# Kernel optimization log

Measured on AMD Instinct MI355X. Metric: run time of the kernel, lower is better.

Reference implementation:

```python
import jax, jax.numpy as jnp
import numpy as np

B, T, D = 32, 1024, 768
H = 768          # GRU hidden size
INNER = 512      # fc output size
NOUT = 39        # out_proj outputs (13 classes x 3 ACCDOA coords)


def setup_inputs() -> dict:
    key = jax.random.key(0)
    ks = jax.random.split(key, 16)
    s_in = 1.0 / np.sqrt(H)
    inp = {
        "features": jax.random.normal(ks[0], (B, T, D), jnp.float32),
        "padding_mask": jnp.zeros((B, T), jnp.bool_),
        # GRU layer 0 (input D -> H), PyTorch gate order [r, z, n]
        "w_ih0": jax.random.uniform(ks[1], (3 * H, D), jnp.float32, -s_in, s_in),
        "w_hh0": jax.random.uniform(ks[2], (3 * H, H), jnp.float32, -s_in, s_in),
        "b_ih0": jax.random.uniform(ks[3], (3 * H,), jnp.float32, -s_in, s_in),
        "b_hh0": jax.random.uniform(ks[4], (3 * H,), jnp.float32, -s_in, s_in),
        # GRU layer 1 (H -> H)
        "w_ih1": jax.random.uniform(ks[5], (3 * H, H), jnp.float32, -s_in, s_in),
        "w_hh1": jax.random.uniform(ks[6], (3 * H, H), jnp.float32, -s_in, s_in),
        "b_ih1": jax.random.uniform(ks[7], (3 * H,), jnp.float32, -s_in, s_in),
        "b_hh1": jax.random.uniform(ks[8], (3 * H,), jnp.float32, -s_in, s_in),
        # fc: hidden -> inner, then SELU
        "fc_w": jax.random.uniform(ks[9], (INNER, H), jnp.float32, -s_in, s_in),
        "fc_b": jax.random.uniform(ks[10], (INNER,), jnp.float32, -s_in, s_in),
        # out_proj: inner -> num_outs, then tanh
        "out_w": jax.random.uniform(ks[11], (NOUT, INNER), jnp.float32, -1.0 / np.sqrt(INNER), 1.0 / np.sqrt(INNER)),
        "out_b": jax.random.uniform(ks[12], (NOUT,), jnp.float32, -1.0 / np.sqrt(INNER), 1.0 / np.sqrt(INNER)),
    }
    return inp


def _gru_layer(x, w_ih, w_hh, b_ih, b_hh):
    # x: [B, T, Din] -> [B, T, H]; PyTorch GRU math, gate order r,z,n
    b, t, _ = x.shape
    h = w_hh.shape[1]
    # precompute input projections for all timesteps in one big GEMM
    x_proj = jnp.einsum('btd,gd->btg', x, w_ih) + b_ih  # [B, T, 3H]

    def step(h_prev, xp):
        gi_r, gi_z, gi_n = jnp.split(xp, 3, axis=-1)
        gh = h_prev @ w_hh.T + b_hh
        gh_r, gh_z, gh_n = jnp.split(gh, 3, axis=-1)
        r = jax.nn.sigmoid(gi_r + gh_r)
        z = jax.nn.sigmoid(gi_z + gh_z)
        n = jnp.tanh(gi_n + r * gh_n)
        h_new = (1.0 - z) * n + z * h_prev
        return h_new, h_new

    h0 = jnp.zeros((b, h), x.dtype)
    _, ys = jax.lax.scan(step, h0, jnp.swapaxes(x_proj, 0, 1))  # ys: [T, B, H]
    return jnp.swapaxes(ys, 0, 1)


def reference(features, padding_mask, w_ih0, w_hh0, b_ih0, b_hh0,
              w_ih1, w_hh1, b_ih1, b_hh1, fc_w, fc_b, out_w, out_b):
    # dropout_input p=0.0 -> identity (eval); padding_mask unused by forward math
    x = _gru_layer(features, w_ih0, w_hh0, b_ih0, b_hh0)
    x = _gru_layer(x, w_ih1, w_hh1, b_ih1, b_hh1)
    x = jax.nn.selu(x @ fc_w.T + fc_b)          # fc + activation_fn='selu'
    x = jnp.tanh(x @ out_w.T + out_b)           # out_proj + out_activation 'tanh'
    return x
```

## Files before the change

### kernel.cpp

```cpp
#include <hip/hip_runtime.h>
#include <cstdint>

typedef float vf2 __attribute__((ext_vector_type(2)));

#define GB_M 128
#define GB_N 64
#define GB_K 16

__global__ __launch_bounds__(256) void gemm_bt_f32(
    const float* __restrict__ A, const float* __restrict__ B,
    const float* __restrict__ bias, float* __restrict__ C,
    int Mc, int N, int K, int tc_shift, int Tfull, int t0, int act)
{
  __shared__ float As[GB_K][GB_M + 4];
  __shared__ float Bs[GB_K][GB_N + 4];
  const int tid = threadIdx.x;
  const int m0 = blockIdx.y * GB_M;
  const int n0 = blockIdx.x * GB_N;
  const int tx = tid & 15;
  const int ty = tid >> 4;

  const int tcmask = (1 << tc_shift) - 1;
  int arow[2];
#pragma unroll
  for (int i = 0; i < 2; i++) {
    int f = tid + i * 256;
    int row = f >> 2;
    int rc = m0 + row;
    arow[i] = (rc >> tc_shift) * Tfull + t0 + (rc & tcmask);
  }
  const int akq = tid & 3;
  const int brow = tid >> 2;
  const int bn = n0 + brow;

  vf2 acc2[4][4];
#pragma unroll
  for (int i = 0; i < 4; i++)
#pragma unroll
    for (int j = 0; j < 4; j++) acc2[i][j] = (vf2)(0.f);

  for (int k0 = 0; k0 < K; k0 += GB_K) {
#pragma unroll
    for (int i = 0; i < 2; i++) {
      int f = tid + i * 256;
      int row = f >> 2;
      float4 v = *(const float4*)(A + (size_t)arow[i] * K + k0 + akq * 4);
      As[akq * 4 + 0][row] = v.x; As[akq * 4 + 1][row] = v.y;
      As[akq * 4 + 2][row] = v.z; As[akq * 4 + 3][row] = v.w;
    }
    {
      float4 v = make_float4(0.f, 0.f, 0.f, 0.f);
      if (bn < N) v = *(const float4*)(B + (size_t)bn * K + k0 + akq * 4);
      Bs[akq * 4 + 0][brow] = v.x; Bs[akq * 4 + 1][brow] = v.y;
      Bs[akq * 4 + 2][brow] = v.z; Bs[akq * 4 + 3][brow] = v.w;
    }
    __syncthreads();
#pragma unroll
    for (int k = 0; k < GB_K; k++) {
      float4 a0 = *(const float4*)&As[k][ty * 8];
      float4 a1 = *(const float4*)&As[k][ty * 8 + 4];
      float4 b0 = *(const float4*)&Bs[k][tx * 4];
      vf2 a2[4];
      a2[0] = (vf2){a0.x, a0.y}; a2[1] = (vf2){a0.z, a0.w};
      a2[2] = (vf2){a1.x, a1.y}; a2[3] = (vf2){a1.z, a1.w};
      float bv[4] = {b0.x, b0.y, b0.z, b0.w};
#pragma unroll
      for (int j = 0; j < 4; j++) {
        vf2 bs = (vf2){bv[j], bv[j]};
#pragma unroll
        for (int ip = 0; ip < 4; ip++)
          acc2[ip][j] = __builtin_elementwise_fma(a2[ip], bs, acc2[ip][j]);
      }
    }
    __syncthreads();
  }

#pragma unroll
  for (int j = 0; j < 4; j++) {
    int n = n0 + tx * 4 + j;
    if (n >= N) continue;
    float bz = bias[n];
#pragma unroll
    for (int i = 0; i < 8; i++) {
      int m = m0 + ty * 8 + i;
      float x = ((i & 1) ? acc2[i >> 1][j].y : acc2[i >> 1][j].x) + bz;
      if (act == 1) {
        x = 1.0507009873554805f * (x > 0.f ? x : 1.6732632423543772f * (__expf(x) - 1.f));
      } else if (act == 2) {
        x = tanhf(x);
      }
      C[(size_t)m * N + n] = x;
    }
  }
}

#define RT 384
#define RNWG 256

__device__ __forceinline__ void pollge(const unsigned* fp, unsigned want) {
  while (__hip_atomic_load(fp, __ATOMIC_RELAXED, __HIP_MEMORY_SCOPE_AGENT) < want)
    __builtin_amdgcn_s_sleep(1);
}

__global__ __launch_bounds__(RT, 1) void gru_rec(
    const float* __restrict__ gi, const float* __restrict__ w_hh,
    const float* __restrict__ b_hh, float* __restrict__ hb,
    unsigned* __restrict__ flags, float* __restrict__ seq,
    int t0, int Tc)
{
  __shared__ float hs[8][776];
  const int wg = blockIdx.x;
  const int jg = wg & 63;
  const int sd = wg >> 6;
  const int j0 = jg * 12;
  const int tid = threadIdx.x;
  const int p  = tid >> 6;
  const int ks = tid & 63;

  unsigned* flagX_my = flags + (((0 * 4 + sd) * 64) + jg) * 16;
  unsigned* flagY_my = flags + (((1 * 4 + sd) * 64) + jg) * 16;

  float4 wreg[3][2][3];
#pragma unroll
  for (int g = 0; g < 3; g++)
#pragma unroll
    for (int j2 = 0; j2 < 2; j2++)
#pragma unroll
      for (int kk = 0; kk < 3; kk++)
        wreg[g][j2][kk] = *(const float4*)(
            w_hh + (size_t)(g * 768 + j0 + 2 * p + j2) * 768 + (kk * 64 + ks) * 4);

  const int j2l = (ks >> 2) & 1;
  const int cl  = ks & 3;
  const int j_out  = j0 + 2 * p + j2l;
  const int bX_out = 8 * sd + cl;
  const int bY_out = 8 * sd + 4 + cl;
  const float bhr = b_hh[j_out];
  const float bhz = b_hh[768 + j_out];
  const float bhn = b_hh[1536 + j_out];

  const int sbi = tid >> 6;
  const int sk  = tid & 63;
  const unsigned* fX_st = flags + (((0 * 4 + sd) * 64) + sk) * 16;
  const unsigned* fY_st = flags + (((1 * 4 + sd) * 64) + sk) * 16;

  const bool hi4 = (ks & 4) != 0;
  const bool hi2 = (ks & 2) != 0;
  const bool hi1 = (ks & 1) != 0;

  for (int tt = 0; tt < Tc; tt++) {
    const int t = t0 + tt;

    float gXr = 0.f, gXz = 0.f, gXn = 0.f;
    if (ks < 8) {
      const float* gX = gi + ((size_t)bX_out * Tc + tt) * 2304 + j_out;
      gXr = gX[0]; gXz = gX[768]; gXn = gX[1536];
    }
    if (tid < 256) {
      pollge(fX_st, (unsigned)t);
      const unsigned long long* src = (const unsigned long long*)
          (hb + (size_t)(t & 1) * 24576 + (size_t)(8 * sd + sbi) * 768) + sk * 6;
      unsigned long long v[6];
#pragma unroll
      for (int i = 0; i < 6; i++)
        v[i] = __hip_atomic_load(src + i, __ATOMIC_RELAXED, __HIP_MEMORY_SCOPE_AGENT);
      float* dst = &hs[sbi][sk * 12];
#pragma unroll
      for (int q = 0; q < 3; q++) {
        *(float4*)(dst + q * 4) = make_float4(
            __uint_as_float((unsigned)v[2 * q]),
            __uint_as_float((unsigned)(v[2 * q] >> 32)),
            __uint_as_float((unsigned)v[2 * q + 1]),
            __uint_as_float((unsigned)(v[2 * q + 1] >> 32)));
      }
    }
    __syncthreads();
    if (tid == 0)
      __hip_atomic_store(flagY_my, (unsigned)t, __ATOMIC_RELAXED, __HIP_MEMORY_SCOPE_AGENT);

    float r3[3];
    {
      vf2 a2[3][2][4];
#pragma unroll
      for (int g = 0; g < 3; g++)
#pragma unroll
        for (int j2 = 0; j2 < 2; j2++)
#pragma unroll
          for (int c = 0; c < 4; c++) a2[g][j2][c] = (vf2)(0.f);
#pragma unroll
      for (int kk = 0; kk < 3; kk++) {
        const int off = (kk * 64 + ks) * 4;
        vf2 hlo[4], hhi[4];
#pragma unroll
        for (int c = 0; c < 4; c++) {
          float4 h = *(const float4*)(&hs[c][0] + off);
          hlo[c] = (vf2){h.x, h.y};
          hhi[c] = (vf2){h.z, h.w};
        }
#pragma unroll
        for (int g = 0; g < 3; g++)
#pragma unroll
          for (int j2 = 0; j2 < 2; j2++) {
            float4 w = wreg[g][j2][kk];
            vf2 wlo = (vf2){w.x, w.y};
            vf2 whi = (vf2){w.z, w.w};
#pragma unroll
            for (int c = 0; c < 4; c++) {
              a2[g][j2][c] = __builtin_elementwise_fma(wlo, hlo[c], a2[g][j2][c]);
              a2[g][j2][c] = __builtin_elementwise_fma(whi, hhi[c], a2[g][j2][c]);
            }
          }
      }
      float acc[3][2][4];
#pragma unroll
      for (int g = 0; g < 3; g++)
#pragma unroll
        for (int j2 = 0; j2 < 2; j2++)
#pragma unroll
          for (int c = 0; c < 4; c++) acc[g][j2][c] = a2[g][j2][c].x + a2[g][j2][c].y;

      float r12[3][4];
#pragma unroll
      for (int g = 0; g < 3; g++)
#pragma unroll
        for (int c = 0; c < 4; c++) {
          float send = hi4 ? acc[g][0][c] : acc[g][1][c];
          float keep = hi4 ? acc[g][1][c] : acc[g][0][c];
          r12[g][c] = keep + __shfl_xor(send, 4);
        }
      float r6[3][2];
#pragma unroll
      for (int g = 0; g < 3; g++)
#pragma unroll
        for (int c2 = 0; c2 < 2; c2++) {
          float send = hi2 ? r12[g][c2] : r12[g][2 + c2];
          float keep = hi2 ? r12[g][2 + c2] : r12[g][c2];
          r6[g][c2] = keep + __shfl_xor(send, 2);
        }
#pragma unroll
      for (int g = 0; g < 3; g++) {
        float send = hi1 ? r6[g][0] : r6[g][1];
        float keep = hi1 ? r6[g][1] : r6[g][0];
        r3[g] = keep + __shfl_xor(send, 1);
      }
#pragma unroll
      for (int g = 0; g < 3; g++) {
        r3[g] += __shfl_xor(r3[g], 8);
        r3[g] += __shfl_xor(r3[g], 16);
        r3[g] += __shfl_xor(r3[g], 32);
      }
    }
    if (ks < 8) {
      float hp = hs[cl][j_out];
      float r = 1.f / (1.f + __expf(-(gXr + r3[0] + bhr)));
      float z = 1.f / (1.f + __expf(-(gXz + r3[1] + bhz)));
      float n = tanhf(gXn + r * (r3[2] + bhn));
      float hv = (1.f - z) * n + z * hp;
      __hip_atomic_store(hb + (size_t)((t + 1) & 1) * 24576 + (size_t)bX_out * 768 + j_out,
                         hv, __ATOMIC_RELAXED, __HIP_MEMORY_SCOPE_AGENT);
      seq[((size_t)bX_out * 1024 + t) * 768 + j_out] = hv;
    }

    float gYr = 0.f, gYz = 0.f, gYn = 0.f;
    if (ks < 8) {
      const float* gY = gi + ((size_t)bY_out * Tc + tt) * 2304 + j_out;
      gYr = gY[0]; gYz = gY[768]; gYn = gY[1536];
    }
    if (tid < 256) {
      pollge(fY_st, (unsigned)t);
      const unsigned long long* src = (const unsigned long long*)
          (hb + (size_t)(t & 1) * 24576 + (size_t)(8 * sd + 4 + sbi) * 768) + sk * 6;
      unsigned long long v[6];
#pragma unroll
      for (int i = 0; i < 6; i++)
        v[i] = __hip_atomic_load(src + i, __ATOMIC_RELAXED, __HIP_MEMORY_SCOPE_AGENT);
      float* dst = &hs[4 + sbi][sk * 12];
#pragma unroll
      for (int q = 0; q < 3; q++) {
        *(float4*)(dst + q * 4) = make_float4(
            __uint_as_float((unsigned)v[2 * q]),
            __uint_as_float((unsigned)(v[2 * q] >> 32)),
            __uint_as_float((unsigned)v[2 * q + 1]),
            __uint_as_float((unsigned)(v[2 * q + 1] >> 32)));
      }
    }
    __syncthreads();
    if (tid == 0)
      __hip_atomic_store(flagX_my, (unsigned)(t + 1), __ATOMIC_RELAXED, __HIP_MEMORY_SCOPE_AGENT);

    {
      vf2 a2[3][2][4];
#pragma unroll
      for (int g = 0; g < 3; g++)
#pragma unroll
        for (int j2 = 0; j2 < 2; j2++)
#pragma unroll
          for (int c = 0; c < 4; c++) a2[g][j2][c] = (vf2)(0.f);
#pragma unroll
      for (int kk = 0; kk < 3; kk++) {
        const int off = (kk * 64 + ks) * 4;
        vf2 hlo[4], hhi[4];
#pragma unroll
        for (int c = 0; c < 4; c++) {
          float4 h = *(const float4*)(&hs[4 + c][0] + off);
          hlo[c] = (vf2){h.x, h.y};
          hhi[c] = (vf2){h.z, h.w};
        }
#pragma unroll
        for (int g = 0; g < 3; g++)
#pragma unroll
          for (int j2 = 0; j2 < 2; j2++) {
            float4 w = wreg[g][j2][kk];
            vf2 wlo = (vf2){w.x, w.y};
            vf2 whi = (vf2){w.z, w.w};
#pragma unroll
            for (int c = 0; c < 4; c++) {
              a2[g][j2][c] = __builtin_elementwise_fma(wlo, hlo[c], a2[g][j2][c]);
              a2[g][j2][c] = __builtin_elementwise_fma(whi, hhi[c], a2[g][j2][c]);
            }
          }
      }
      float acc[3][2][4];
#pragma unroll
      for (int g = 0; g < 3; g++)
#pragma unroll
        for (int j2 = 0; j2 < 2; j2++)
#pragma unroll
          for (int c = 0; c < 4; c++) acc[g][j2][c] = a2[g][j2][c].x + a2[g][j2][c].y;

      float r12[3][4];
#pragma unroll
      for (int g = 0; g < 3; g++)
#pragma unroll
        for (int c = 0; c < 4; c++) {
          float send = hi4 ? acc[g][0][c] : acc[g][1][c];
          float keep = hi4 ? acc[g][1][c] : acc[g][0][c];
          r12[g][c] = keep + __shfl_xor(send, 4);
        }
      float r6[3][2];
#pragma unroll
      for (int g = 0; g < 3; g++)
#pragma unroll
        for (int c2 = 0; c2 < 2; c2++) {
          float send = hi2 ? r12[g][c2] : r12[g][2 + c2];
          float keep = hi2 ? r12[g][2 + c2] : r12[g][c2];
          r6[g][c2] = keep + __shfl_xor(send, 2);
        }
#pragma unroll
      for (int g = 0; g < 3; g++) {
        float send = hi1 ? r6[g][0] : r6[g][1];
        float keep = hi1 ? r6[g][1] : r6[g][0];
        r3[g] = keep + __shfl_xor(send, 1);
      }
#pragma unroll
      for (int g = 0; g < 3; g++) {
        r3[g] += __shfl_xor(r3[g], 8);
        r3[g] += __shfl_xor(r3[g], 16);
        r3[g] += __shfl_xor(r3[g], 32);
      }
    }
    if (ks < 8) {
      float hp = hs[4 + cl][j_out];
      float r = 1.f / (1.f + __expf(-(gYr + r3[0] + bhr)));
      float z = 1.f / (1.f + __expf(-(gYz + r3[1] + bhz)));
      float n = tanhf(gYn + r * (r3[2] + bhn));
      float hv = (1.f - z) * n + z * hp;
      __hip_atomic_store(hb + (size_t)((t + 1) & 1) * 24576 + (size_t)bY_out * 768 + j_out,
                         hv, __ATOMIC_RELAXED, __HIP_MEMORY_SCOPE_AGENT);
      seq[((size_t)bY_out * 1024 + t) * 768 + j_out] = hv;
    }
  }
  __syncthreads();
  if (tid == 0)
    __hip_atomic_store(flagY_my, (unsigned)(t0 + Tc), __ATOMIC_RELAXED, __HIP_MEMORY_SCOPE_AGENT);
}

extern "C" void kernel_launch(void* const* d_in, const int* in_sizes, int n_in,
                              void* d_out, int out_size, void* d_ws, size_t ws_size,
                              hipStream_t stream) {
  const float* feat  = (const float*)d_in[0];
  const float* w_ih0 = (const float*)d_in[2];
  const float* w_hh0 = (const float*)d_in[3];
  const float* b_ih0 = (const float*)d_in[4];
  const float* b_hh0 = (const float*)d_in[5];
  const float* w_ih1 = (const float*)d_in[6];
  const float* w_hh1 = (const float*)d_in[7];
  const float* b_ih1 = (const float*)d_in[8];
  const float* b_hh1 = (const float*)d_in[9];
  const float* fc_w  = (const float*)d_in[10];
  const float* fc_b  = (const float*)d_in[11];
  const float* out_w = (const float*)d_in[12];
  const float* out_b = (const float*)d_in[13];
  float* out = (float*)d_out;

  const int Tc = 256;
  const int McChunk = 32 * Tc;
  const size_t DYN_LDS = 65536;

  float* proj = (float*)d_ws;
  float* seq  = proj + (size_t)32 * Tc * 2304;
  float* hbuf = seq + (size_t)25165824;
  unsigned* flags = (unsigned*)(hbuf + 2 * 24576);

  hipMemsetAsync(hbuf, 0, 2 * 24576 * sizeof(float), stream);
  hipMemsetAsync(flags, 0, 32768, stream);
  for (int c = 0; c < 4; c++) {
    gemm_bt_f32<<<dim3(36, McChunk / 128), dim3(256), 0, stream>>>(
        feat, w_ih0, b_ih0, proj, McChunk, 2304, 768, 8, 1024, c * Tc, 0);
    gru_rec<<<dim3(RNWG), dim3(RT), DYN_LDS, stream>>>(
        proj, w_hh0, b_hh0, hbuf, flags, seq, c * Tc, Tc);
  }
  hipMemsetAsync(hbuf, 0, 2 * 24576 * sizeof(float), stream);
  hipMemsetAsync(flags, 0, 32768, stream);
  for (int c = 0; c < 4; c++) {
    gemm_bt_f32<<<dim3(36, McChunk / 128), dim3(256), 0, stream>>>(
        seq, w_ih1, b_ih1, proj, McChunk, 2304, 768, 8, 1024, c * Tc, 0);
    gru_rec<<<dim3(RNWG), dim3(RT), DYN_LDS, stream>>>(
        proj, w_hh1, b_hh1, hbuf, flags, seq, c * Tc, Tc);
  }
  gemm_bt_f32<<<dim3(8, 256), dim3(256), 0, stream>>>(
      seq, fc_w, fc_b, proj, 32768, 512, 768, 15, 32768, 0, 1);
  gemm_bt_f32<<<dim3(1, 256), dim3(256), 0, stream>>>(
      proj, out_w, out_b, out, 32768, 39, 512, 15, 32768, 0, 2);
}
```

Baseline: 12.88 ms.

## Wavefront-pipeline the two GRU layers in one persistent recurrent launch

Merges the layer-0 and layer-1 recurrent kernels into a single launch of 512 workgroups. Layer 1 processes time chunk c-1 while layer 0 processes chunk c, so the two serial recurrences overlap in a diagonal schedule. Each layer gets its own projection, sequence, hidden-state and flag buffers, and the input GEMMs are interleaved between recurrent launches. This doubles the number of resident spin-waiting workgroups (launch bounds raised to 3 per CU) and uses more workspace. Co-residency is required to avoid deadlock, and layer 1 now competes with layer 0 for bandwidth and CU time.

```diff
diff --git a/kernel.cpp b/kernel.cpp
--- a/kernel.cpp
+++ b/kernel.cpp
@@ -95,21 +95,18 @@
 }
 
 #define RT 384
-#define RNWG 256
 
 __device__ __forceinline__ void pollge(const unsigned* fp, unsigned want) {
   while (__hip_atomic_load(fp, __ATOMIC_RELAXED, __HIP_MEMORY_SCOPE_AGENT) < want)
     __builtin_amdgcn_s_sleep(1);
 }
 
-__global__ __launch_bounds__(RT, 1) void gru_rec(
+__device__ __forceinline__ void rec_body(
     const float* __restrict__ gi, const float* __restrict__ w_hh,
     const float* __restrict__ b_hh, float* __restrict__ hb,
     unsigned* __restrict__ flags, float* __restrict__ seq,
-    int t0, int Tc)
+    int t0, int Tc, int wg, float (*hs)[776])
 {
-  __shared__ float hs[8][776];
-  const int wg = blockIdx.x;
   const int jg = wg & 63;
   const int sd = wg >> 6;
   const int j0 = jg * 12;
@@ -373,6 +370,28 @@
   __syncthreads();
   if (tid == 0)
     __hip_atomic_store(flagY_my, (unsigned)(t0 + Tc), __ATOMIC_RELAXED, __HIP_MEMORY_SCOPE_AGENT);
+}
+
+__global__ __launch_bounds__(RT, 3) void gru_rec2(
+    const float* __restrict__ gi0, const float* __restrict__ w_hh0,
+    const float* __restrict__ b_hh0, float* __restrict__ hb0,
+    unsigned* __restrict__ flags0, float* __restrict__ seq0,
+    const float* __restrict__ gi1, const float* __restrict__ w_hh1,
+    const float* __restrict__ b_hh1, float* __restrict__ hb1,
+    unsigned* __restrict__ flags1, float* __restrict__ seq1,
+    int t0a, int Tc, int enA, int enB)
+{
+  __shared__ float hs[8][776];
+  const int bid = blockIdx.x;
+  const int fam = bid >> 8;
+  const int wg = bid & 255;
+  if (fam == 0) {
+    if (!enA) return;
+    rec_body(gi0, w_hh0, b_hh0, hb0, flags0, seq0, t0a, Tc, wg, hs);
+  } else {
+    if (!enB) return;
+    rec_body(gi1, w_hh1, b_hh1, hb1, flags1, seq1, t0a - 256, Tc, wg, hs);
+  }
 }
 
 extern "C" void kernel_launch(void* const* d_in, const int* in_sizes, int n_in,
@@ -394,32 +413,43 @@
   float* out = (float*)d_out;
 
   const int Tc = 256;
-  const int McChunk = 32 * Tc;
-  const size_t DYN_LDS = 65536;
-
-  float* proj = (float*)d_ws;
-  float* seq  = proj + (size_t)32 * Tc * 2304;
-  float* hbuf = seq + (size_t)25165824;
-  unsigned* flags = (unsigned*)(hbuf + 2 * 24576);
-
-  hipMemsetAsync(hbuf, 0, 2 * 24576 * sizeof(float), stream);
-  hipMemsetAsync(flags, 0, 32768, stream);
-  for (int c = 0; c < 4; c++) {
-    gemm_bt_f32<<<dim3(36, McChunk / 128), dim3(256), 0, stream>>>(
-        feat, w_ih0, b_ih0, proj, McChunk, 2304, 768, 8, 1024, c * Tc, 0);
-    gru_rec<<<dim3(RNWG), dim3(RT), DYN_LDS, stream>>>(
-        proj, w_hh0, b_hh0, hbuf, flags, seq, c * Tc, Tc);
-  }
-  hipMemsetAsync(hbuf, 0, 2 * 24576 * sizeof(float), stream);
-  hipMemsetAsync(flags, 0, 32768, stream);
-  for (int c = 0; c < 4; c++) {
-    gemm_bt_f32<<<dim3(36, McChunk / 128), dim3(256), 0, stream>>>(
-        seq, w_ih1, b_ih1, proj, McChunk, 2304, 768, 8, 1024, c * Tc, 0);
-    gru_rec<<<dim3(RNWG), dim3(RT), DYN_LDS, stream>>>(
-        proj, w_hh1, b_hh1, hbuf, flags, seq, c * Tc, Tc);
-  }
+  const size_t PROJ = (size_t)32 * Tc * 2304;
+  const size_t SEQ  = (size_t)32 * 1024 * 768;
+
+  float* proj0 = (float*)d_ws;
+  float* proj1 = proj0 + PROJ;
+  float* seq0  = proj1 + PROJ;
+  float* seq1  = seq0 + SEQ;
+  float* hb0   = seq1 + SEQ;
+  float* hb1   = hb0 + 2 * 24576;
+  unsigned* flags0 = (unsigned*)(hb1 + 2 * 24576);
+  unsigned* flags1 = flags0 + 8192;
+
+  hipMemsetAsync(hb0, 0, 4 * 24576 * sizeof(float), stream);
+  hipMemsetAsync(flags0, 0, 65536, stream);
+
+  auto G0 = [&](int c) {
+    gemm_bt_f32<<<dim3(36, 64), dim3(256), 0, stream>>>(
+        feat, w_ih0, b_ih0, proj0, 8192, 2304, 768, 8, 1024, c * Tc, 0);
+  };
+  auto G1 = [&](int c) {
+    gemm_bt_f32<<<dim3(36, 64), dim3(256), 0, stream>>>(
+        seq0, w_ih1, b_ih1, proj1, 8192, 2304, 768, 8, 1024, c * Tc, 0);
+  };
+  auto R = [&](int t0a, int eA, int eB) {
+    gru_rec2<<<dim3(512), dim3(RT), 0, stream>>>(
+        proj0, w_hh0, b_hh0, hb0, flags0, seq0,
+        proj1, w_hh1, b_hh1, hb1, flags1, seq1, t0a, Tc, eA, eB);
+  };
+
+  G0(0);        R(0, 1, 0);
+  G0(1); G1(0); R(256, 1, 1);
+  G0(2); G1(1); R(512, 1, 1);
+  G0(3); G1(2); R(768, 1, 1);
+  G1(3);        R(1024, 0, 1);
+
   gemm_bt_f32<<<dim3(8, 256), dim3(256), 0, stream>>>(
-      seq, fc_w, fc_b, proj, 32768, 512, 768, 15, 32768, 0, 1);
+      seq1, fc_w, fc_b, proj0, 32768, 512, 768, 15, 32768, 0, 1);
   gemm_bt_f32<<<dim3(1, 256), dim3(256), 0, stream>>>(
-      proj, out_w, out_b, out, 32768, 39, 512, 15, 32768, 0, 2);
+      proj0, out_w, out_b, out, 32768, 39, 512, 15, 32768, 0, 2);
 }
```

Result: slower. 16.97 ms (+31.8%).

## Replace flag-based inter-workgroup sync with step-tagged hidden-state words

Applied to the files above, without the earlier changes.

Each hidden-state value is now stored as a 64-bit word that packs the float with its timestep tag, so consumers poll the data itself instead of separate per-workgroup flags. This removes the flag stores, the extra flag-polling round trip and the anti-dependency (Y) flags, shortening the critical path of each recurrent step. It doubles the bytes read per hidden vector and changes the load pattern to strided 64-bit loads. Dropping the reader-done flags relies on the double buffer never being overwritten before every reader has consumed it. The dynamic LDS request is also removed.

```diff
diff --git a/kernel.cpp b/kernel.cpp
--- a/kernel.cpp
+++ b/kernel.cpp
@@ -97,16 +97,10 @@
 #define RT 384
 #define RNWG 256
 
-__device__ __forceinline__ void pollge(const unsigned* fp, unsigned want) {
-  while (__hip_atomic_load(fp, __ATOMIC_RELAXED, __HIP_MEMORY_SCOPE_AGENT) < want)
-    __builtin_amdgcn_s_sleep(1);
-}
-
 __global__ __launch_bounds__(RT, 1) void gru_rec(
     const float* __restrict__ gi, const float* __restrict__ w_hh,
-    const float* __restrict__ b_hh, float* __restrict__ hb,
-    unsigned* __restrict__ flags, float* __restrict__ seq,
-    int t0, int Tc)
+    const float* __restrict__ b_hh, unsigned long long* __restrict__ gx,
+    float* __restrict__ seq, int t0, int Tc)
 {
   __shared__ float hs[8][776];
   const int wg = blockIdx.x;
@@ -117,9 +111,6 @@
   const int p  = tid >> 6;
   const int ks = tid & 63;
 
-  unsigned* flagX_my = flags + (((0 * 4 + sd) * 64) + jg) * 16;
-  unsigned* flagY_my = flags + (((1 * 4 + sd) * 64) + jg) * 16;
-
   float4 wreg[3][2][3];
 #pragma unroll
   for (int g = 0; g < 3; g++)
@@ -141,8 +132,6 @@
 
   const int sbi = tid >> 6;
   const int sk  = tid & 63;
-  const unsigned* fX_st = flags + (((0 * 4 + sd) * 64) + sk) * 16;
-  const unsigned* fY_st = flags + (((1 * 4 + sd) * 64) + sk) * 16;
 
   const bool hi4 = (ks & 4) != 0;
   const bool hi2 = (ks & 2) != 0;
@@ -150,6 +139,7 @@
 
   for (int tt = 0; tt < Tc; tt++) {
     const int t = t0 + tt;
+    const unsigned wantt = (unsigned)t;
 
     float gXr = 0.f, gXz = 0.f, gXn = 0.f;
     if (ks < 8) {
@@ -157,26 +147,29 @@
       gXr = gX[0]; gXz = gX[768]; gXn = gX[1536];
     }
     if (tid < 256) {
-      pollge(fX_st, (unsigned)t);
-      const unsigned long long* src = (const unsigned long long*)
-          (hb + (size_t)(t & 1) * 24576 + (size_t)(8 * sd + sbi) * 768) + sk * 6;
-      unsigned long long v[6];
-#pragma unroll
-      for (int i = 0; i < 6; i++)
-        v[i] = __hip_atomic_load(src + i, __ATOMIC_RELAXED, __HIP_MEMORY_SCOPE_AGENT);
-      float* dst = &hs[sbi][sk * 12];
-#pragma unroll
-      for (int q = 0; q < 3; q++) {
-        *(float4*)(dst + q * 4) = make_float4(
-            __uint_as_float((unsigned)v[2 * q]),
-            __uint_as_float((unsigned)(v[2 * q] >> 32)),
-            __uint_as_float((unsigned)v[2 * q + 1]),
-            __uint_as_float((unsigned)(v[2 * q + 1] >> 32)));
-      }
+      const unsigned long long* src =
+          gx + (size_t)(t & 1) * 24576 + (size_t)(8 * sd + sbi) * 768 + sk;
+      unsigned long long v[12];
+#pragma unroll
+      for (int i = 0; i < 12; i++)
+        v[i] = __hip_atomic_load(src + 64 * i, __ATOMIC_RELAXED, __HIP_MEMORY_SCOPE_AGENT);
+      while (true) {
+        unsigned miss = 0;
+#pragma unroll
+        for (int i = 0; i < 12; i++)
+          miss |= (unsigned)((unsigned)(v[i] >> 32) < wantt);
+        if (!miss) break;
+        __builtin_amdgcn_s_sleep(1);
+#pragma unroll
+        for (int i = 0; i < 12; i++)
+          if ((unsigned)(v[i] >> 32) < wantt)
+            v[i] = __hip_atomic_load(src + 64 * i, __ATOMIC_RELAXED, __HIP_MEMORY_SCOPE_AGENT);
+      }
+#pragma unroll
+      for (int i = 0; i < 12; i++)
+        hs[sbi][sk + 64 * i] = __uint_as_float((unsigned)v[i]);
     }
     __syncthreads();
-    if (tid == 0)
-      __hip_atomic_store(flagY_my, (unsigned)t, __ATOMIC_RELAXED, __HIP_MEMORY_SCOPE_AGENT);
 
     float r3[3];
     {
@@ -256,8 +249,11 @@
       float z = 1.f / (1.f + __expf(-(gXz + r3[1] + bhz)));
       float n = tanhf(gXn + r * (r3[2] + bhn));
       float hv = (1.f - z) * n + z * hp;
-      __hip_atomic_store(hb + (size_t)((t + 1) & 1) * 24576 + (size_t)bX_out * 768 + j_out,
-                         hv, __ATOMIC_RELAXED, __HIP_MEMORY_SCOPE_AGENT);
+      __hip_atomic_store(
+          gx + (size_t)((t + 1) & 1) * 24576 + (size_t)bX_out * 768 + j_out,
+          ((unsigned long long)(unsigned)(t + 1) << 32) |
+              (unsigned long long)__float_as_uint(hv),
+          __ATOMIC_RELAXED, __HIP_MEMORY_SCOPE_AGENT);
       seq[((size_t)bX_out * 1024 + t) * 768 + j_out] = hv;
     }
 
@@ -267,26 +263,29 @@
       gYr = gY[0]; gYz = gY[768]; gYn = gY[1536];
     }
     if (tid < 256) {
-      pollge(fY_st, (unsigned)t);
-      const unsigned long long* src = (const unsigned long long*)
-          (hb + (size_t)(t & 1) * 24576 + (size_t)(8 * sd + 4 + sbi) * 768) + sk * 6;
-      unsigned long long v[6];
-#pragma unroll
-      for (int i = 0; i < 6; i++)
-        v[i] = __hip_atomic_load(src + i, __ATOMIC_RELAXED, __HIP_MEMORY_SCOPE_AGENT);
-      float* dst = &hs[4 + sbi][sk * 12];
-#pragma unroll
-      for (int q = 0; q < 3; q++) {
-        *(float4*)(dst + q * 4) = make_float4(
-            __uint_as_float((unsigned)v[2 * q]),
-            __uint_as_float((unsigned)(v[2 * q] >> 32)),
-            __uint_as_float((unsigned)v[2 * q + 1]),
-            __uint_as_float((unsigned)(v[2 * q + 1] >> 32)));
-      }
+      const unsigned long long* src =
+          gx + (size_t)(t & 1) * 24576 + (size_t)(8 * sd + 4 + sbi) * 768 + sk;
+      unsigned long long v[12];
+#pragma unroll
+      for (int i = 0; i < 12; i++)
+        v[i] = __hip_atomic_load(src + 64 * i, __ATOMIC_RELAXED, __HIP_MEMORY_SCOPE_AGENT);
+      while (true) {
+        unsigned miss = 0;
+#pragma unroll
+        for (int i = 0; i < 12; i++)
+          miss |= (unsigned)((unsigned)(v[i] >> 32) < wantt);
+        if (!miss) break;
+        __builtin_amdgcn_s_sleep(1);
+#pragma unroll
+        for (int i = 0; i < 12; i++)
+          if ((unsigned)(v[i] >> 32) < wantt)
+            v[i] = __hip_atomic_load(src + 64 * i, __ATOMIC_RELAXED, __HIP_MEMORY_SCOPE_AGENT);
+      }
+#pragma unroll
+      for (int i = 0; i < 12; i++)
+        hs[4 + sbi][sk + 64 * i] = __uint_as_float((unsigned)v[i]);
     }
     __syncthreads();
-    if (tid == 0)
-      __hip_atomic_store(flagX_my, (unsigned)(t + 1), __ATOMIC_RELAXED, __HIP_MEMORY_SCOPE_AGENT);
 
     {
       vf2 a2[3][2][4];
@@ -365,14 +364,14 @@
       float z = 1.f / (1.f + __expf(-(gYz + r3[1] + bhz)));
       float n = tanhf(gYn + r * (r3[2] + bhn));
       float hv = (1.f - z) * n + z * hp;
-      __hip_atomic_store(hb + (size_t)((t + 1) & 1) * 24576 + (size_t)bY_out * 768 + j_out,
-                         hv, __ATOMIC_RELAXED, __HIP_MEMORY_SCOPE_AGENT);
+      __hip_atomic_store(
+          gx + (size_t)((t + 1) & 1) * 24576 + (size_t)bY_out * 768 + j_out,
+          ((unsigned long long)(unsigned)(t + 1) << 32) |
+              (unsigned long long)__float_as_uint(hv),
+          __ATOMIC_RELAXED, __HIP_MEMORY_SCOPE_AGENT);
       seq[((size_t)bY_out * 1024 + t) * 768 + j_out] = hv;
     }
   }
-  __syncthreads();
-  if (tid == 0)
-    __hip_atomic_store(flagY_my, (unsigned)(t0 + Tc), __ATOMIC_RELAXED, __HIP_MEMORY_SCOPE_AGENT);
 }
 
 extern "C" void kernel_launch(void* const* d_in, const int* in_sizes, int n_in,
@@ -395,28 +394,25 @@
 
   const int Tc = 256;
   const int McChunk = 32 * Tc;
-  const size_t DYN_LDS = 65536;
 
   float* proj = (float*)d_ws;
   float* seq  = proj + (size_t)32 * Tc * 2304;
-  float* hbuf = seq + (size_t)25165824;
-  unsigned* flags = (unsigned*)(hbuf + 2 * 24576);
-
-  hipMemsetAsync(hbuf, 0, 2 * 24576 * sizeof(float), stream);
-  hipMemsetAsync(flags, 0, 32768, stream);
+  unsigned long long* gx = (unsigned long long*)(seq + (size_t)25165824);
+  const size_t GXB = (size_t)2 * 24576 * 8;
+
+  hipMemsetAsync(gx, 0, GXB, stream);
   for (int c = 0; c < 4; c++) {
     gemm_bt_f32<<<dim3(36, McChunk / 128), dim3(256), 0, stream>>>(
         feat, w_ih0, b_ih0, proj, McChunk, 2304, 768, 8, 1024, c * Tc, 0);
-    gru_rec<<<dim3(RNWG), dim3(RT), DYN_LDS, stream>>>(
-        proj, w_hh0, b_hh0, hbuf, flags, seq, c * Tc, Tc);
-  }
-  hipMemsetAsync(hbuf, 0, 2 * 24576 * sizeof(float), stream);
-  hipMemsetAsync(flags, 0, 32768, stream);
+    gru_rec<<<dim3(RNWG), dim3(RT), 0, stream>>>(
+        proj, w_hh0, b_hh0, gx, seq, c * Tc, Tc);
+  }
+  hipMemsetAsync(gx, 0, GXB, stream);
   for (int c = 0; c < 4; c++) {
     gemm_bt_f32<<<dim3(36, McChunk / 128), dim3(256), 0, stream>>>(
         seq, w_ih1, b_ih1, proj, McChunk, 2304, 768, 8, 1024, c * Tc, 0);
-    gru_rec<<<dim3(RNWG), dim3(RT), DYN_LDS, stream>>>(
-        proj, w_hh1, b_hh1, hbuf, flags, seq, c * Tc, Tc);
+    gru_rec<<<dim3(RNWG), dim3(RT), 0, stream>>>(
+        proj, w_hh1, b_hh1, gx, seq, c * Tc, Tc);
   }
   gemm_bt_f32<<<dim3(8, 256), dim3(256), 0, stream>>>(
       seq, fc_w, fc_b, proj, 32768, 512, 768, 15, 32768, 0, 1);
```

Result: faster. 12.29 ms (-4.6%).
